# Kernel tuning notes

Measured on AMD Instinct MI355X. Metric: run time of the kernel, lower is better.

The kernel has to match this reference:

```python
import jax, jax.numpy as jnp
import numpy as np

N = 65536
APP = 1024
SP = 512
HID = 512
CARD = 16
SUB = HID // CARD  # 32


def setup_inputs() -> dict:
    key = jax.random.key(0)
    ks = jax.random.split(key, 8)
    s1 = 1.0 / np.sqrt(APP)
    s2 = 1.0 / np.sqrt(SP)
    s3 = 1.0 / np.sqrt(SUB)
    return {
        "appearance": jax.random.normal(ks[0], (N, APP), jnp.float32),
        "spatial": jax.random.normal(ks[1], (N, SP), jnp.float32),
        # Batched per-branch weights (torch Linear: y = x @ W.T + b; here stored as [in, out])
        "W1": jax.random.uniform(ks[2], (CARD, APP, SUB), jnp.float32, -s1, s1),
        "b1": jax.random.uniform(ks[3], (CARD, SUB), jnp.float32, -s1, s1),
        "W2": jax.random.uniform(ks[4], (CARD, SP, SUB), jnp.float32, -s2, s2),
        "b2": jax.random.uniform(ks[5], (CARD, SP if False else SUB), jnp.float32, -s2, s2),
        "W3": jax.random.uniform(ks[6], (CARD, SUB, HID), jnp.float32, -s3, s3),
        "b3": jax.random.uniform(ks[7], (CARD, HID), jnp.float32, -s3, s3),
    }


def reference(appearance, spatial, W1, b1, W2, b2, W3, b3):
    # fc1[c] = appearance @ W1[c] + b1[c]; fc2[c] = spatial @ W2[c] + b2[c]
    h1 = jnp.einsum('na,cas->ncs', appearance, W1) + b1[None]  # [N, C, SUB]
    h2 = jnp.einsum('np,cps->ncs', spatial, W2) + b2[None]     # [N, C, SUB]
    h = jax.nn.relu(h1 + h2)
    # sum over branches of (h[:,c] @ W3[c] + b3[c]) == einsum + sum of biases
    out = jnp.einsum('ncs,csh->nh', h, W3) + jnp.sum(b3, axis=0)[None]  # [N, HID]
    return jax.nn.relu(out)
```

## Files before the change

### kernel.cpp

```cpp
#include <hip/hip_runtime.h>

typedef __attribute__((ext_vector_type(4))) float floatx4;
typedef __attribute__((ext_vector_type(8))) short bf16x8;

__device__ __forceinline__ unsigned short f2bf(float f) {
    union { float f; unsigned u; } v; v.f = f;
    unsigned r = v.u + 0x7fffu + ((v.u >> 16) & 1u);
    return (unsigned short)(r >> 16);
}

__global__ void prep_kernel(const float* __restrict__ W1, const float* __restrict__ b1,
                            const float* __restrict__ W2, const float* __restrict__ b2,
                            const float* __restrict__ W3, const float* __restrict__ b3,
                            unsigned short* __restrict__ wcat, unsigned short* __restrict__ w3f,
                            float* __restrict__ bias12, float* __restrict__ bias3s)
{
    int tid = blockIdx.x * 256 + threadIdx.x;
    if (tid < 98304) {
        int l  = tid & 63;
        int nt = (tid >> 6) & 31;
        int kc = tid >> 11;
        int n  = nt * 16 + (l & 15);
        int k0 = kc * 32 + ((l >> 4) << 3);
        int c = n >> 5, s = n & 31;
        union { unsigned short us[8]; int4 v; } pk;
        const float* src = (k0 < 1024) ? (W1 + c * 32768 + k0 * 32 + s)
                                       : (W2 + c * 16384 + (k0 - 1024) * 32 + s);
        #pragma unroll
        for (int j = 0; j < 8; ++j) pk.us[j] = f2bf(src[j * 32]);
        *(int4*)(wcat + (size_t)tid * 8) = pk.v;
    } else if (tid < 131072) {
        int t  = tid - 98304;
        int l  = t & 63;
        int nt = (t >> 6) & 31;
        int kc = t >> 11;
        int n  = nt * 16 + (l & 15);
        int k0 = kc * 32 + ((l >> 4) << 3);
        union { unsigned short us[8]; int4 v; } pk;
        const float* src = W3 + k0 * 512 + n;
        #pragma unroll
        for (int j = 0; j < 8; ++j) pk.us[j] = f2bf(src[j * 512]);
        *(int4*)(w3f + (size_t)t * 8) = pk.v;
    } else if (tid < 131584) {
        int n = tid - 131072;
        bias12[n] = b1[n] + b2[n];
        float sacc = 0.f;
        #pragma unroll
        for (int c = 0; c < 16; ++c) sacc += b3[c * 512 + n];
        bias3s[n] = sacc;
    }
}

__global__ __launch_bounds__(512, 4) void fused_main(
    const float* __restrict__ app, const float* __restrict__ sp,
    const unsigned short* __restrict__ wcat, const unsigned short* __restrict__ w3f,
    const float* __restrict__ bias12, const float* __restrict__ bias3s,
    float* __restrict__ out)
{
    __shared__ unsigned short As[2][4][64][8];
    __shared__ unsigned short Hf[4][16][64][8];

    const int tid = (int)threadIdx.x;
    const int w   = tid >> 6;
    const int l   = tid & 63;
    const int rowbase = (int)blockIdx.x * 64;

    const int sr  = tid >> 3;
    const int scc = tid & 7;
    const float* appsrc = app + (size_t)(rowbase + sr) * 1024 + scc * 4;
    const float* spsrc  = sp  + (size_t)(rowbase + sr) * 512  + scc * 4;
    unsigned short* as0 = &As[0][sr >> 4][(scc >> 1) * 16 + (sr & 15)][(scc & 1) * 4];
    unsigned short* as1 = &As[1][sr >> 4][(scc >> 1) * 16 + (sr & 15)][(scc & 1) * 4];

    floatx4 acc[4][4];
    #pragma unroll
    for (int mt = 0; mt < 4; ++mt)
        #pragma unroll
        for (int nt = 0; nt < 4; ++nt)
            acc[mt][nt] = (floatx4){0.f, 0.f, 0.f, 0.f};

    {
        float4 p = *(const float4*)(appsrc);
        union { unsigned short us[4]; int2 v; } pk;
        pk.us[0] = f2bf(p.x); pk.us[1] = f2bf(p.y);
        pk.us[2] = f2bf(p.z); pk.us[3] = f2bf(p.w);
        *(int2*)as0 = pk.v;
    }
    float4 pA = *(const float4*)(appsrc + 32);

    for (int kb = 0; kb < 48; ++kb) {
        __syncthreads();
        const int buf = kb & 1;
        float4 pB;
        if (kb + 2 < 48) {
            const float* src = (kb + 2 < 32) ? (appsrc + (kb + 2) * 32)
                                             : (spsrc + (kb + 2 - 32) * 32);
            pB = *(const float4*)src;
        }
        bf16x8 bfrag[4];
        #pragma unroll
        for (int nt = 0; nt < 4; ++nt)
            bfrag[nt] = *(const bf16x8*)(wcat + (((size_t)kb * 32 + w * 4 + nt) * 64 + l) * 8);
        bf16x8 afrag[4];
        #pragma unroll
        for (int mt = 0; mt < 4; ++mt)
            afrag[mt] = *(const bf16x8*)(&As[buf][mt][l][0]);
        #pragma unroll
        for (int mt = 0; mt < 4; ++mt)
            #pragma unroll
            for (int nt = 0; nt < 4; ++nt)
                acc[mt][nt] = __builtin_amdgcn_mfma_f32_16x16x32_bf16(
                    afrag[mt], bfrag[nt], acc[mt][nt], 0, 0, 0);
        if (kb + 1 < 48) {
            union { unsigned short us[4]; int2 v; } pk;
            pk.us[0] = f2bf(pA.x); pk.us[1] = f2bf(pA.y);
            pk.us[2] = f2bf(pA.z); pk.us[3] = f2bf(pA.w);
            *(int2*)((buf == 0) ? as1 : as0) = pk.v;
            pA = pB;
        }
    }

    #pragma unroll
    for (int nt = 0; nt < 4; ++nt) {
        const int colg = w * 64 + nt * 16 + (l & 15);
        const float bv = bias12[colg];
        const int kc  = colg >> 5;
        const int lhi = ((colg >> 3) & 3) << 4;
        const int j   = colg & 7;
        #pragma unroll
        for (int mt = 0; mt < 4; ++mt)
            #pragma unroll
            for (int r = 0; r < 4; ++r) {
                const int rlow = ((l >> 4) << 2) + r;
                float v = acc[mt][nt][r] + bv;
                v = fmaxf(v, 0.f);
                Hf[mt][kc][lhi + rlow][j] = f2bf(v);
            }
    }
    __syncthreads();

    #pragma unroll
    for (int mt = 0; mt < 4; ++mt)
        #pragma unroll
        for (int nt = 0; nt < 4; ++nt)
            acc[mt][nt] = (floatx4){0.f, 0.f, 0.f, 0.f};

    for (int kc = 0; kc < 16; ++kc) {
        bf16x8 bfrag[4];
        #pragma unroll
        for (int nt = 0; nt < 4; ++nt)
            bfrag[nt] = *(const bf16x8*)(w3f + (((size_t)kc * 32 + w * 4 + nt) * 64 + l) * 8);
        bf16x8 afrag[4];
        #pragma unroll
        for (int mt = 0; mt < 4; ++mt)
            afrag[mt] = *(const bf16x8*)(&Hf[mt][kc][l][0]);
        #pragma unroll
        for (int mt = 0; mt < 4; ++mt)
            #pragma unroll
            for (int nt = 0; nt < 4; ++nt)
                acc[mt][nt] = __builtin_amdgcn_mfma_f32_16x16x32_bf16(
                    afrag[mt], bfrag[nt], acc[mt][nt], 0, 0, 0);
    }

    #pragma unroll
    for (int nt = 0; nt < 4; ++nt) {
        const int colg = w * 64 + nt * 16 + (l & 15);
        const float bv = bias3s[colg];
        #pragma unroll
        for (int mt = 0; mt < 4; ++mt)
            #pragma unroll
            for (int r = 0; r < 4; ++r) {
                const int rowg = mt * 16 + ((l >> 4) << 2) + r;
                float v = acc[mt][nt][r] + bv;
                v = fmaxf(v, 0.f);
                out[(size_t)(rowbase + rowg) * 512 + colg] = v;
            }
    }
}

extern "C" void kernel_launch(void* const* d_in, const int* in_sizes, int n_in,
                              void* d_out, int out_size, void* d_ws, size_t ws_size,
                              hipStream_t stream)
{
    const float* app = (const float*)d_in[0];
    const float* sp  = (const float*)d_in[1];
    const float* W1  = (const float*)d_in[2];
    const float* b1  = (const float*)d_in[3];
    const float* W2  = (const float*)d_in[4];
    const float* b2  = (const float*)d_in[5];
    const float* W3  = (const float*)d_in[6];
    const float* b3  = (const float*)d_in[7];

    char* ws = (char*)d_ws;
    unsigned short* wcat  = (unsigned short*)(ws);
    unsigned short* w3f   = (unsigned short*)(ws + 1572864);
    float*          b12   = (float*)(ws + 2097152);
    float*          b3s   = (float*)(ws + 2099200);

    prep_kernel<<<514, 256, 0, stream>>>(W1, b1, W2, b2, W3, b3, wcat, w3f, b12, b3s);

    float* outp = (float*)d_out;
    fused_main<<<65536 / 64, 512, 0, stream>>>(app, sp, wcat, w3f, b12, b3s, outp);
}
```

Baseline: 564.0 us.

## Software-pipeline weight fragment loads and replace syncthreads with lgkm-only barriers

The weight B-fragments for both GEMM phases are now prefetched one k-step ahead in registers, with each next-step load issued right after the MFMAs that consume the current fragment. The LDS A-fragment read and the staging store are moved before the MFMAs in each iteration. __syncthreads is replaced by an s_waitcnt lgkmcnt(0) plus a raw s_barrier, so the barrier no longer waits on outstanding global loads. The goal is to hide global-load latency behind MFMA work, at the cost of more live registers and reliance on hand-placed LDS hazard handling.

```diff
diff --git a/kernel.cpp b/kernel.cpp
--- a/kernel.cpp
+++ b/kernel.cpp
@@ -88,37 +88,61 @@
     }
     float4 pA = *(const float4*)(appsrc + 32);
 
+    const unsigned short* wbase = wcat + (size_t)w * 2048 + (size_t)l * 8;
+    bf16x8 bcur[4];
+    #pragma unroll
+    for (int nt = 0; nt < 4; ++nt)
+        bcur[nt] = *(const bf16x8*)(wbase + nt * 512);
+
+    asm volatile("s_waitcnt lgkmcnt(0)" ::: "memory");
+    __builtin_amdgcn_s_barrier();
+    asm volatile("" ::: "memory");
+
     for (int kb = 0; kb < 48; ++kb) {
-        __syncthreads();
-        const int buf = kb & 1;
+        bf16x8 af[4];
+        #pragma unroll
+        for (int mt = 0; mt < 4; ++mt)
+            af[mt] = *(const bf16x8*)(&As[kb & 1][mt][l][0]);
+
         float4 pB;
         if (kb + 2 < 48) {
             const float* src = (kb + 2 < 32) ? (appsrc + (kb + 2) * 32)
-                                             : (spsrc + (kb + 2 - 32) * 32);
+                                             : (spsrc + (kb - 30) * 32);
             pB = *(const float4*)src;
         }
-        bf16x8 bfrag[4];
-        #pragma unroll
-        for (int nt = 0; nt < 4; ++nt)
-            bfrag[nt] = *(const bf16x8*)(wcat + (((size_t)kb * 32 + w * 4 + nt) * 64 + l) * 8);
-        bf16x8 afrag[4];
-        #pragma unroll
-        for (int mt = 0; mt < 4; ++mt)
-            afrag[mt] = *(const bf16x8*)(&As[buf][mt][l][0]);
-        #pragma unroll
-        for (int mt = 0; mt < 4; ++mt)
-            #pragma unroll
-            for (int nt = 0; nt < 4; ++nt)
-                acc[mt][nt] = __builtin_amdgcn_mfma_f32_16x16x32_bf16(
-                    afrag[mt], bfrag[nt], acc[mt][nt], 0, 0, 0);
+
         if (kb + 1 < 48) {
             union { unsigned short us[4]; int2 v; } pk;
             pk.us[0] = f2bf(pA.x); pk.us[1] = f2bf(pA.y);
             pk.us[2] = f2bf(pA.z); pk.us[3] = f2bf(pA.w);
-            *(int2*)((buf == 0) ? as1 : as0) = pk.v;
-            pA = pB;
-        }
-    }
+            *(int2*)(((kb & 1) == 0) ? as1 : as0) = pk.v;
+        }
+
+        const unsigned short* wp = wbase + (size_t)(kb + 1) * 16384;
+        #pragma unroll
+        for (int nt = 0; nt < 4; ++nt) {
+            #pragma unroll
+            for (int mt = 0; mt < 4; ++mt)
+                acc[mt][nt] = __builtin_amdgcn_mfma_f32_16x16x32_bf16(
+                    af[mt], bcur[nt], acc[mt][nt], 0, 0, 0);
+            if (kb + 1 < 48)
+                bcur[nt] = *(const bf16x8*)(wp + nt * 512);
+        }
+
+        pA = pB;
+
+        if (kb + 1 < 48) {
+            asm volatile("s_waitcnt lgkmcnt(0)" ::: "memory");
+            __builtin_amdgcn_s_barrier();
+            asm volatile("" ::: "memory");
+        }
+    }
+
+    const unsigned short* w3base = w3f + (size_t)w * 2048 + (size_t)l * 8;
+    bf16x8 b3[4];
+    #pragma unroll
+    for (int nt = 0; nt < 4; ++nt)
+        b3[nt] = *(const bf16x8*)(w3base + nt * 512);
 
     #pragma unroll
     for (int nt = 0; nt < 4; ++nt) {
@@ -137,7 +161,9 @@
                 Hf[mt][kc][lhi + rlow][j] = f2bf(v);
             }
     }
-    __syncthreads();
+    asm volatile("s_waitcnt lgkmcnt(0)" ::: "memory");
+    __builtin_amdgcn_s_barrier();
+    asm volatile("" ::: "memory");
 
     #pragma unroll
     for (int mt = 0; mt < 4; ++mt)
@@ -146,20 +172,20 @@
             acc[mt][nt] = (floatx4){0.f, 0.f, 0.f, 0.f};
 
     for (int kc = 0; kc < 16; ++kc) {
-        bf16x8 bfrag[4];
-        #pragma unroll
-        for (int nt = 0; nt < 4; ++nt)
-            bfrag[nt] = *(const bf16x8*)(w3f + (((size_t)kc * 32 + w * 4 + nt) * 64 + l) * 8);
-        bf16x8 afrag[4];
-        #pragma unroll
-        for (int mt = 0; mt < 4; ++mt)
-            afrag[mt] = *(const bf16x8*)(&Hf[mt][kc][l][0]);
-        #pragma unroll
-        for (int mt = 0; mt < 4; ++mt)
-            #pragma unroll
-            for (int nt = 0; nt < 4; ++nt)
+        bf16x8 af[4];
+        #pragma unroll
+        for (int mt = 0; mt < 4; ++mt)
+            af[mt] = *(const bf16x8*)(&Hf[mt][kc][l][0]);
+        const unsigned short* wp = w3base + (size_t)(kc + 1) * 16384;
+        #pragma unroll
+        for (int nt = 0; nt < 4; ++nt) {
+            #pragma unroll
+            for (int mt = 0; mt < 4; ++mt)
                 acc[mt][nt] = __builtin_amdgcn_mfma_f32_16x16x32_bf16(
-                    afrag[mt], bfrag[nt], acc[mt][nt], 0, 0, 0);
+                    af[mt], b3[nt], acc[mt][nt], 0, 0, 0);
+            if (kc + 1 < 16)
+                b3[nt] = *(const bf16x8*)(wp + nt * 512);
+        }
     }
 
     #pragma unroll
```

Result: slower. 581.6 us (+3.1%).
